# Optimization experiments

Hardware: AMD Instinct MI355X
Metric: run time of the kernel (lower is better)

The kernel has to match this reference:

```python
import jax, jax.numpy as jnp
import numpy as np

ROT_DIM = 32
THETA = 10000.0
HEAD_SIZE = 192


def _rope(t):
    # t: [B, T, D]; rotate first ROT_DIM features with interleaved-pair RoPE
    T = t.shape[1]
    inv_freq = 1.0 / (THETA ** (jnp.arange(0, ROT_DIM, 2, dtype=jnp.float32) / ROT_DIM))  # [16]
    freqs = jnp.arange(T, dtype=jnp.float32)[:, None] * inv_freq[None, :]  # [T,16]
    freqs = jnp.repeat(freqs, 2, axis=-1)  # [T,32], each freq repeated for the pair
    cos = jnp.cos(freqs).astype(t.dtype)
    sin = jnp.sin(freqs).astype(t.dtype)
    x = t[..., :ROT_DIM]
    x1 = x[..., 0::2]
    x2 = x[..., 1::2]
    rot_half = jnp.stack([-x2, x1], axis=-1).reshape(x.shape)  # interleave (-x2, x1)
    rotated = x * cos + rot_half * sin
    return jnp.concatenate([rotated, t[..., ROT_DIM:]], axis=-1)


def setup_inputs() -> dict:
    key = jax.random.key(0)
    k1, k2, k3, k4 = jax.random.split(key, 4)
    B, T, C, H = 64, 512, 768, HEAD_SIZE
    x = jax.random.normal(k1, (B, T, C), dtype=jnp.float32)
    s = 1.0 / np.sqrt(C)
    Wq = jax.random.normal(k2, (C, H), dtype=jnp.float32) * s
    Wk = jax.random.normal(k3, (C, H), dtype=jnp.float32) * s
    Wv = jax.random.normal(k4, (C, H), dtype=jnp.float32) * s
    return {"x": x, "Wq": Wq, "Wk": Wk, "Wv": Wv}


def reference(x, Wq, Wk, Wv):
    B, T, C = x.shape
    q = x @ Wq  # [B,T,H]
    k = x @ Wk
    v = x @ Wv
    q = _rope(q)
    k = _rope(k)
    scale = k.shape[-1] ** -0.5
    scores = jnp.einsum('bqh,bkh->bqk', q, k) * scale  # [B,T,T]
    causal = jnp.tril(jnp.ones((T, T), dtype=bool))
    scores = jnp.where(causal[None, :, :], scores, -jnp.inf)
    weight = jax.nn.softmax(scores, axis=-1)
    # dropout is identity at eval time
    out = jnp.einsum('bqk,bkh->bqh', weight, v)  # [B,T,H]
    return out
```

## Files before the change

kernel.cpp:

```cpp
#include <hip/hip_runtime.h>
#include <cstdint>

typedef __attribute__((ext_vector_type(8))) short short8;
typedef __attribute__((ext_vector_type(4))) float floatx4;

__device__ __forceinline__ unsigned short f2bf(float f) {
  uint32_t u = __builtin_bit_cast(uint32_t, f);
  u += 0x7fffu + ((u >> 16) & 1u);
  return (unsigned short)(u >> 16);
}
__device__ __forceinline__ uint32_t pkbf(float lo, float hi) {
  uint32_t a = __builtin_bit_cast(uint32_t, lo) + 0x8000u;
  uint32_t b = __builtin_bit_cast(uint32_t, hi) + 0x8000u;
  return __builtin_amdgcn_perm(b, a, 0x07060302);
}
__device__ __forceinline__ void gll16(const void* g, void* l) {
  __builtin_amdgcn_global_load_lds(
      (const __attribute__((address_space(1))) unsigned int*)g,
      (__attribute__((address_space(3))) unsigned int*)l, 16, 0, 0);
}

__global__ void prep_w_kernel(const float* __restrict__ Wq,
                              const float* __restrict__ Wk,
                              const float* __restrict__ Wv,
                              unsigned short* __restrict__ Wt) {
  int id = blockIdx.x * 256 + threadIdx.x;
  int bz = id / 18432, rem = id - bz * 18432;
  int kb = rem / 768, s = rem - kb * 768;
  int row = s >> 2, cs = s & 3;
  int c = cs ^ ((row >> 1) & 3);
  const float* W = (bz == 0) ? Wq : (bz == 1) ? Wk : Wv;
  int k0 = kb * 32 + c * 8;
  unsigned short v[8];
#pragma unroll
  for (int e = 0; e < 8; ++e) v[e] = f2bf(W[(size_t)(k0 + e) * 192 + row]);
  uint4 o;
  o.x = v[0] | ((uint32_t)v[1] << 16);
  o.y = v[2] | ((uint32_t)v[3] << 16);
  o.z = v[4] | ((uint32_t)v[5] << 16);
  o.w = v[6] | ((uint32_t)v[7] << 16);
  *(uint4*)(Wt + (size_t)id * 8) = o;
}

__global__ __launch_bounds__(256, 3) void proj_kernel(
    const float* __restrict__ x, const unsigned short* __restrict__ Wt,
    unsigned short* __restrict__ q_ws, unsigned short* __restrict__ k_ws,
    unsigned short* __restrict__ v_ws) {
  __shared__ __align__(16) unsigned short A_lds[3][64 * 32];
  __shared__ __align__(16) unsigned short B_lds[3][192 * 32];
  const int tid = threadIdx.x;
  const int w = tid >> 6, l = tid & 63, quad = l >> 4, ln = l & 15;
  const int wr = w & 1, wc = w >> 1;
  const int m0 = blockIdx.x * 64;
  const int bz = blockIdx.y;

  const int arow = tid >> 2, ac = tid & 3;
  const int aslot = ((ac ^ ((arow >> 1) & 3)) << 4);
  const float* xp = x + (size_t)(m0 + arow) * 768 + ac * 8;
  const unsigned short* wimg = Wt + (size_t)bz * 18432 * 8;

  const int fq = ((quad ^ ((ln >> 1) & 3)) << 4);

  floatx4 acc[2][6];
#pragma unroll
  for (int mi = 0; mi < 2; ++mi)
#pragma unroll
    for (int nj = 0; nj < 6; ++nj) acc[mi][nj] = floatx4{0.f, 0.f, 0.f, 0.f};

  float4 ax0, ay0, ax1, ay1, ax2, ay2;

#define LOADA(S, K0)                               \
  do {                                             \
    ax##S = *(const float4*)(xp + (K0));           \
    ay##S = *(const float4*)(xp + (K0) + 4);       \
  } while (0)
#define STAGEA(S, AB)                                             \
  do {                                                            \
    uint4 ap;                                                     \
    ap.x = pkbf(ax##S.x, ax##S.y);                                \
    ap.y = pkbf(ax##S.z, ax##S.w);                                \
    ap.z = pkbf(ay##S.x, ay##S.y);                                \
    ap.w = pkbf(ay##S.z, ay##S.w);                                \
    *(uint4*)((char*)&A_lds[AB][0] + arow * 64 + aslot) = ap;     \
  } while (0)
#define DMAB(KB1, BB)                                             \
  do {                                                            \
    const unsigned short* src = wimg + (size_t)(KB1)*6144;        \
    char* dstb = (char*)&B_lds[BB][0];                            \
    gll16(src + tid * 8, dstb + tid * 16);                        \
    gll16(src + (256 + tid) * 8, dstb + (256 + tid) * 16);        \
    gll16(src + (512 + tid) * 8, dstb + (512 + tid) * 16);        \
  } while (0)
#define WAITBAR(N)                                                          \
  asm volatile("s_waitcnt vmcnt(" #N ") lgkmcnt(0)\n\ts_barrier" ::: "memory")
#define PCOMPUTE(C)                                                              \
  do {                                                                           \
    short8 af0 = *(const short8*)((const char*)&A_lds[C][0] +                    \
                                  (wr * 32 + ln) * 64 + fq);                     \
    short8 af1 = *(const short8*)((const char*)&A_lds[C][0] +                    \
                                  (wr * 32 + 16 + ln) * 64 + fq);                \
    _Pragma("unroll") for (int nj = 0; nj < 6; ++nj) {                           \
      short8 bf = *(const short8*)((const char*)&B_lds[C][0] +                   \
                                   (wc * 96 + nj * 16 + ln) * 64 + fq);          \
      acc[0][nj] = __builtin_amdgcn_mfma_f32_16x16x32_bf16(af0, bf, acc[0][nj],  \
                                                           0, 0, 0);             \
      acc[1][nj] = __builtin_amdgcn_mfma_f32_16x16x32_bf16(af1, bf, acc[1][nj],  \
                                                           0, 0, 0);             \
    }                                                                            \
  } while (0)
#define BODY(KB, C, P)            \
  do {                            \
    STAGEA(P, P);                 \
    DMAB((KB) + 1, P);            \
    LOADA(C, ((KB) + 3) * 32);    \
    WAITBAR(7);                   \
    PCOMPUTE(C);                  \
  } while (0)

  DMAB(0, 0);
  LOADA(0, 0);
  LOADA(1, 32);
  LOADA(2, 64);
  STAGEA(0, 0);

  BODY(0, 0, 1);
  for (int t = 1; t <= 16; t += 3) {
    BODY(t, 1, 2);
    BODY(t + 1, 2, 0);
    BODY(t + 2, 0, 1);
  }
  BODY(19, 1, 2);
  BODY(20, 2, 0);
  { STAGEA(1, 1); DMAB(22, 1); WAITBAR(5); PCOMPUTE(0); }
  { STAGEA(2, 2); DMAB(23, 2); WAITBAR(3); PCOMPUTE(1); }
  { WAITBAR(0); PCOMPUTE(2); }

#undef LOADA
#undef STAGEA
#undef DMAB
#undef WAITBAR
#undef PCOMPUTE
#undef BODY

  const float R_LG = 0.8304820237218406f;
#define ROPE2(V0, V1, TPOS)                                         \
  do {                                                              \
    float i0 = (float)(ln >> 1);                                    \
    float f0 = exp2f(-i0 * R_LG);                                   \
    float f1 = exp2f(-(i0 + 8.0f) * R_LG);                          \
    float s0, c0, s1, c1;                                           \
    sincosf((float)(TPOS)*f0, &s0, &c0);                            \
    sincosf((float)(TPOS)*f1, &s1, &c1);                            \
    float p0 = __shfl_xor(V0, 1), p1 = __shfl_xor(V1, 1);           \
    V0 = (ln & 1) ? (V0 * c0 + p0 * s0) : (V0 * c0 - p0 * s0);      \
    V1 = (ln & 1) ? (V1 * c1 + p1 * s1) : (V1 * c1 - p1 * s1);      \
  } while (0)

  if (bz < 2) {
    unsigned short* dst = (bz == 0) ? q_ws : k_ws;
    if (wc == 0) {
#pragma unroll
      for (int mi = 0; mi < 2; ++mi)
#pragma unroll
        for (int r = 0; r < 4; ++r) {
          int row_g = m0 + wr * 32 + mi * 16 + quad * 4 + r;
          int t_pos = row_g & 511;
          float v0 = acc[mi][0][r], v1 = acc[mi][1][r];
          ROPE2(v0, v1, t_pos);
          dst[(size_t)row_g * 192 + ln] = f2bf(v0);
          dst[(size_t)row_g * 192 + 16 + ln] = f2bf(v1);
#pragma unroll
          for (int nj = 2; nj < 6; ++nj)
            dst[(size_t)row_g * 192 + nj * 16 + ln] = f2bf(acc[mi][nj][r]);
        }
    } else {
#pragma unroll
      for (int mi = 0; mi < 2; ++mi)
#pragma unroll
        for (int r = 0; r < 4; ++r) {
          int row_g = m0 + wr * 32 + mi * 16 + quad * 4 + r;
#pragma unroll
          for (int nj = 0; nj < 6; ++nj)
            dst[(size_t)row_g * 192 + 96 + nj * 16 + ln] = f2bf(acc[mi][nj][r]);
        }
    }
  } else {
    const int dbase = wc * 96;
#pragma unroll
    for (int mi = 0; mi < 2; ++mi) {
      int rb = m0 + wr * 32 + mi * 16 + quad * 4;
      int bb = rb >> 9, t = rb & 511;
#pragma unroll
      for (int nj = 0; nj < 6; ++nj) {
        ushort4 pv;
        pv.x = f2bf(acc[mi][nj][0]);
        pv.y = f2bf(acc[mi][nj][1]);
        pv.z = f2bf(acc[mi][nj][2]);
        pv.w = f2bf(acc[mi][nj][3]);
        *(ushort4*)&v_ws[((size_t)bb * 192 + dbase + nj * 16 + ln) * 512 + t] = pv;
      }
    }
  }
#undef ROPE2
}

__global__ __launch_bounds__(256) void attn_kernel(
    const unsigned short* __restrict__ q_ws, const unsigned short* __restrict__ k_ws,
    const unsigned short* __restrict__ v_ws, float* __restrict__ out) {
  __shared__ __align__(16) unsigned short K_lds[64 * 200];
  __shared__ __align__(16) unsigned short V_lds[192 * 72];
  __shared__ __align__(16) unsigned short P_lds[4][16 * 72];
  const int tid = threadIdx.x;
  const int w = tid >> 6, l = tid & 63, quad = l >> 4, ln = l & 15;
  const int b = blockIdx.y;
  const int qt = (blockIdx.y < 32) ? blockIdx.x : 7 - blockIdx.x;
  const int q0 = qt * 64;

  short8 qf[6];
  {
    const unsigned short* qp =
        q_ws + (size_t)(b * 512 + q0 + w * 16 + ln) * 192 + quad * 8;
#pragma unroll
    for (int kk = 0; kk < 6; ++kk) qf[kk] = *(const short8*)(qp + kk * 32);
  }

  float m_i[4], l_i[4];
  floatx4 o[12];
#pragma unroll
  for (int r = 0; r < 4; ++r) { m_i[r] = -1e30f; l_i[r] = 0.f; }
#pragma unroll
  for (int nt = 0; nt < 12; ++nt) o[nt] = floatx4{0.f, 0.f, 0.f, 0.f};
  const float sm_scale = 0.07216878364870323f;

  for (int kt = 0; kt <= qt; ++kt) {
    const int k0 = kt * 64;
    __syncthreads();
#pragma unroll
    for (int it = 0; it < 6; ++it) {
      int idx = it * 256 + tid;
      int row = idx / 24, c = idx - row * 24;
      uint4 v = *(const uint4*)(k_ws + (size_t)(b * 512 + k0 + row) * 192 + c * 8);
      *(uint4*)&K_lds[row * 200 + c * 8] = v;
    }
#pragma unroll
    for (int it = 0; it < 6; ++it) {
      int idx = it * 256 + tid;
      int row = idx >> 3, c = idx & 7;
      uint4 v = *(const uint4*)(v_ws + (size_t)(b * 192 + row) * 512 + k0 + c * 8);
      *(uint4*)&V_lds[row * 72 + c * 8] = v;
    }
    __syncthreads();

    float s[4][4];
    __builtin_amdgcn_s_setprio(1);
#pragma unroll
    for (int nt = 0; nt < 4; ++nt) {
      floatx4 sa = floatx4{0.f, 0.f, 0.f, 0.f};
#pragma unroll
      for (int kk = 0; kk < 6; ++kk) {
        short8 kf = *(const short8*)&K_lds[(nt * 16 + ln) * 200 + kk * 32 + quad * 8];
        sa = __builtin_amdgcn_mfma_f32_16x16x32_bf16(qf[kk], kf, sa, 0, 0, 0);
      }
#pragma unroll
      for (int r = 0; r < 4; ++r) s[nt][r] = sa[r] * sm_scale;
    }
    __builtin_amdgcn_s_setprio(0);
    if (kt == qt) {
#pragma unroll
      for (int nt = 0; nt < 4; ++nt)
#pragma unroll
        for (int r = 0; r < 4; ++r)
          if (nt * 16 + ln > w * 16 + quad * 4 + r) s[nt][r] = -1e30f;
    }
    float alpha[4];
#pragma unroll
    for (int r = 0; r < 4; ++r) {
      float mx = fmaxf(fmaxf(s[0][r], s[1][r]), fmaxf(s[2][r], s[3][r]));
      mx = fmaxf(mx, __shfl_xor(mx, 1));
      mx = fmaxf(mx, __shfl_xor(mx, 2));
      mx = fmaxf(mx, __shfl_xor(mx, 4));
      mx = fmaxf(mx, __shfl_xor(mx, 8));
      float mnew = fmaxf(m_i[r], mx);
      alpha[r] = __expf(m_i[r] - mnew);
      float sum = 0.f;
#pragma unroll
      for (int nt = 0; nt < 4; ++nt) {
        s[nt][r] = __expf(s[nt][r] - mnew);
        sum += s[nt][r];
      }
      sum += __shfl_xor(sum, 1);
      sum += __shfl_xor(sum, 2);
      sum += __shfl_xor(sum, 4);
      sum += __shfl_xor(sum, 8);
      l_i[r] = l_i[r] * alpha[r] + sum;
      m_i[r] = mnew;
    }
#pragma unroll
    for (int nt = 0; nt < 12; ++nt)
#pragma unroll
      for (int r = 0; r < 4; ++r) o[nt][r] *= alpha[r];

#pragma unroll
    for (int nt = 0; nt < 4; ++nt)
#pragma unroll
      for (int r = 0; r < 4; ++r)
        P_lds[w][(quad * 4 + r) * 72 + nt * 16 + ln] = f2bf(s[nt][r]);
    __asm__ volatile("s_waitcnt lgkmcnt(0)" ::: "memory");

    __builtin_amdgcn_s_setprio(1);
#pragma unroll
    for (int ks = 0; ks < 2; ++ks) {
      short8 pf = *(const short8*)&P_lds[w][ln * 72 + ks * 32 + quad * 8];
#pragma unroll
      for (int nt = 0; nt < 12; ++nt) {
        short8 vf = *(const short8*)&V_lds[(nt * 16 + ln) * 72 + ks * 32 + quad * 8];
        o[nt] = __builtin_amdgcn_mfma_f32_16x16x32_bf16(pf, vf, o[nt], 0, 0, 0);
      }
    }
    __builtin_amdgcn_s_setprio(0);
  }

#pragma unroll
  for (int r = 0; r < 4; ++r) {
    float inv = 1.0f / l_i[r];
    size_t rowoff = (size_t)(b * 512 + q0 + w * 16 + quad * 4 + r) * 192;
#pragma unroll
    for (int nt = 0; nt < 12; ++nt)
      out[rowoff + nt * 16 + ln] = o[nt][r] * inv;
  }
}

extern "C" void kernel_launch(void* const* d_in, const int* in_sizes, int n_in,
                              void* d_out, int out_size, void* d_ws, size_t ws_size,
                              hipStream_t stream) {
  const float* x = (const float*)d_in[0];
  const float* Wq = (const float*)d_in[1];
  const float* Wk = (const float*)d_in[2];
  const float* Wv = (const float*)d_in[3];
  float* out = (float*)d_out;

  char* ws = (char*)d_ws;
  const size_t QKV_BYTES = (size_t)64 * 512 * 192 * 2;
  unsigned short* q_ws = (unsigned short*)(ws);
  unsigned short* k_ws = (unsigned short*)(ws + QKV_BYTES);
  unsigned short* v_ws = (unsigned short*)(ws + 2 * QKV_BYTES);
  unsigned short* Wt = (unsigned short*)(ws + 3 * QKV_BYTES);

  hipLaunchKernelGGL(prep_w_kernel, dim3(216), dim3(256), 0, stream, Wq, Wk, Wv, Wt);
  hipLaunchKernelGGL(proj_kernel, dim3(512, 3), dim3(256), 0, stream, x, Wt, q_ws, k_ws, v_ws);
  hipLaunchKernelGGL(attn_kernel, dim3(8, 64), dim3(256), 0, stream, q_ws, k_ws, v_ws, out);
}
```

Measured before the change: 222.5 us.

## Pre-convert x to bf16 for DMA projection and shrink attention key tile to 32

Adds a prep kernel that converts x to bf16 once. A new projection kernel then streams both operands straight into LDS with global_load_lds, in place of register-staged fp32 loads that are converted inside the main loop. This path runs only when the workspace is large enough, and it adds an extra pass over x plus a bf16 copy. Separately, the attention kernel now uses 32-key tiles instead of 64, which halves LDS use and lets the causal diagonal skip finer-grained work, at the cost of twice as many loop iterations and barriers.

New measurement: 236.2 us. 6.2% more time.

```diff
diff --git a/kernel.cpp b/kernel.cpp
--- a/kernel.cpp
+++ b/kernel.cpp
@@ -42,6 +42,151 @@
   *(uint4*)(Wt + (size_t)id * 8) = o;
 }
 
+__global__ void prep_x_kernel(const float* __restrict__ x,
+                              unsigned short* __restrict__ xb) {
+  size_t id = (size_t)blockIdx.x * 256 + threadIdx.x;
+  float4 f0 = *(const float4*)(x + id * 8);
+  float4 f1 = *(const float4*)(x + id * 8 + 4);
+  uint4 o;
+  o.x = pkbf(f0.x, f0.y);
+  o.y = pkbf(f0.z, f0.w);
+  o.z = pkbf(f1.x, f1.y);
+  o.w = pkbf(f1.z, f1.w);
+  *(uint4*)(xb + id * 8) = o;
+}
+
+#define PROJ_EPILOGUE                                                          \
+  const float R_LG = 0.8304820237218406f;                  \
+  if (bz < 2) {                                                                \
+    unsigned short* dst = (bz == 0) ? q_ws : k_ws;                             \
+    if (wc == 0) {                                                             \
+      _Pragma("unroll") for (int mi = 0; mi < 2; ++mi)                         \
+      _Pragma("unroll") for (int r = 0; r < 4; ++r) {                          \
+        int row_g = m0 + wr * 32 + mi * 16 + quad * 4 + r;                     \
+        int t_pos = row_g & 511;                                               \
+        float v0 = acc[mi][0][r], v1 = acc[mi][1][r];                          \
+        {                                                                      \
+          float i0 = (float)(ln >> 1);                                         \
+          float f0 = exp2f(-i0 * R_LG);                                        \
+          float f1 = exp2f(-(i0 + 8.0f) * R_LG);                               \
+          float s0, c0, s1, c1;                                                \
+          sincosf((float)t_pos * f0, &s0, &c0);                                \
+          sincosf((float)t_pos * f1, &s1, &c1);                                \
+          float p0 = __shfl_xor(v0, 1), p1 = __shfl_xor(v1, 1);                \
+          v0 = (ln & 1) ? (v0 * c0 + p0 * s0) : (v0 * c0 - p0 * s0);           \
+          v1 = (ln & 1) ? (v1 * c1 + p1 * s1) : (v1 * c1 - p1 * s1);           \
+        }                                                                      \
+        dst[(size_t)row_g * 192 + ln] = f2bf(v0);                              \
+        dst[(size_t)row_g * 192 + 16 + ln] = f2bf(v1);                         \
+        _Pragma("unroll") for (int nj = 2; nj < 6; ++nj)                       \
+            dst[(size_t)row_g * 192 + nj * 16 + ln] = f2bf(acc[mi][nj][r]);    \
+      }                                                                        \
+    } else {                                                                   \
+      _Pragma("unroll") for (int mi = 0; mi < 2; ++mi)                         \
+      _Pragma("unroll") for (int r = 0; r < 4; ++r) {                          \
+        int row_g = m0 + wr * 32 + mi * 16 + quad * 4 + r;                     \
+        _Pragma("unroll") for (int nj = 0; nj < 6; ++nj)                       \
+            dst[(size_t)row_g * 192 + 96 + nj * 16 + ln] =                     \
+                f2bf(acc[mi][nj][r]);                                          \
+      }                                                                        \
+    }                                                                          \
+  } else {                                                                     \
+    const int dbase = wc * 96;                                                 \
+    _Pragma("unroll") for (int mi = 0; mi < 2; ++mi) {                         \
+      int rb = m0 + wr * 32 + mi * 16 + quad * 4;                              \
+      int bb = rb >> 9, t = rb & 511;                                          \
+      _Pragma("unroll") for (int nj = 0; nj < 6; ++nj) {                       \
+        ushort4 pv;                                                            \
+        pv.x = f2bf(acc[mi][nj][0]);                                           \
+        pv.y = f2bf(acc[mi][nj][1]);                                           \
+        pv.z = f2bf(acc[mi][nj][2]);                                           \
+        pv.w = f2bf(acc[mi][nj][3]);                                           \
+        *(ushort4*)&v_ws[((size_t)bb * 192 + dbase + nj * 16 + ln) * 512 + t] = pv; \
+      }                                                                        \
+    }                                                                          \
+  }
+
+__global__ __launch_bounds__(256, 3) void proj_dma_kernel(
+    const unsigned short* __restrict__ xb, const unsigned short* __restrict__ Wt,
+    unsigned short* __restrict__ q_ws, unsigned short* __restrict__ k_ws,
+    unsigned short* __restrict__ v_ws) {
+  __shared__ __align__(16) unsigned short A_lds[3][64 * 32];
+  __shared__ __align__(16) unsigned short B_lds[3][192 * 32];
+  const int tid = threadIdx.x;
+  const int w = tid >> 6, l = tid & 63, quad = l >> 4, ln = l & 15;
+  const int wr = w & 1, wc = w >> 1;
+  const int m0 = blockIdx.x * 64;
+  const int bz = blockIdx.y;
+
+  const int arow = tid >> 2, ac = tid & 3;
+  const int aswz = ac ^ ((arow >> 1) & 3);
+  const unsigned short* xsrc = xb + (size_t)(m0 + arow) * 768 + aswz * 8;
+  const unsigned short* wimg = Wt + (size_t)bz * 18432 * 8;
+
+  const int fq = ((quad ^ ((ln >> 1) & 3)) << 4);
+
+  floatx4 acc[2][6];
+#pragma unroll
+  for (int mi = 0; mi < 2; ++mi)
+#pragma unroll
+    for (int nj = 0; nj < 6; ++nj) acc[mi][nj] = floatx4{0.f, 0.f, 0.f, 0.f};
+
+#define DMAA(KB, BB) gll16(xsrc + (KB) * 32, (char*)&A_lds[BB][0] + tid * 16)
+#define DMAB(KB, BB)                                                  \
+  do {                                                                \
+    const unsigned short* src = wimg + (size_t)(KB)*6144;             \
+    char* dstb = (char*)&B_lds[BB][0];                                \
+    gll16(src + tid * 8, dstb + tid * 16);                            \
+    gll16(src + (256 + tid) * 8, dstb + (256 + tid) * 16);            \
+    gll16(src + (512 + tid) * 8, dstb + (512 + tid) * 16);            \
+  } while (0)
+#define WAITBAR4 \
+  asm volatile("s_waitcnt vmcnt(4) lgkmcnt(0)\n\ts_barrier" ::: "memory")
+#define WAITBAR0 \
+  asm volatile("s_waitcnt vmcnt(0) lgkmcnt(0)\n\ts_barrier" ::: "memory")
+#define PCOMPUTE(C)                                                              \
+  do {                                                                           \
+    short8 af0 = *(const short8*)((const char*)&A_lds[C][0] +                    \
+                                  (wr * 32 + ln) * 64 + fq);                     \
+    short8 af1 = *(const short8*)((const char*)&A_lds[C][0] +                    \
+                                  (wr * 32 + 16 + ln) * 64 + fq);                \
+    _Pragma("unroll") for (int nj = 0; nj < 6; ++nj) {                           \
+      short8 bf = *(const short8*)((const char*)&B_lds[C][0] +                   \
+                                   (wc * 96 + nj * 16 + ln) * 64 + fq);          \
+      acc[0][nj] = __builtin_amdgcn_mfma_f32_16x16x32_bf16(af0, bf, acc[0][nj],  \
+                                                           0, 0, 0);             \
+      acc[1][nj] = __builtin_amdgcn_mfma_f32_16x16x32_bf16(af1, bf, acc[1][nj],  \
+                                                           0, 0, 0);             \
+    }                                                                            \
+  } while (0)
+#define BODY(J, C, N)                                   \
+  do {                                                  \
+    DMAA((J) + 1, N);                                   \
+    DMAB((J) + 1, N);                                   \
+    WAITBAR4;                                           \
+    PCOMPUTE(C);                                        \
+  } while (0)
+
+  DMAA(0, 0);
+  DMAB(0, 0);
+  BODY(0, 0, 1);
+  for (int t = 1; t <= 19; t += 3) {
+    BODY(t, 1, 2);
+    BODY(t + 1, 2, 0);
+    BODY(t + 2, 0, 1);
+  }
+  BODY(22, 1, 2);
+  { WAITBAR0; PCOMPUTE(2); }
+#undef DMAA
+#undef DMAB
+#undef WAITBAR4
+#undef WAITBAR0
+#undef PCOMPUTE
+#undef BODY
+
+  PROJ_EPILOGUE
+}
+
 __global__ __launch_bounds__(256, 3) void proj_kernel(
     const float* __restrict__ x, const unsigned short* __restrict__ Wt,
     unsigned short* __restrict__ q_ws, unsigned short* __restrict__ k_ws,
@@ -58,7 +203,6 @@
   const int aslot = ((ac ^ ((arow >> 1) & 3)) << 4);
   const float* xp = x + (size_t)(m0 + arow) * 768 + ac * 8;
   const unsigned short* wimg = Wt + (size_t)bz * 18432 * 8;
-
   const int fq = ((quad ^ ((ln >> 1) & 3)) << 4);
 
   floatx4 acc[2][6];
@@ -134,7 +278,6 @@
   { STAGEA(1, 1); DMAB(22, 1); WAITBAR(5); PCOMPUTE(0); }
   { STAGEA(2, 2); DMAB(23, 2); WAITBAR(3); PCOMPUTE(1); }
   { WAITBAR(0); PCOMPUTE(2); }
-
 #undef LOADA
 #undef STAGEA
 #undef DMAB
@@ -142,74 +285,15 @@
 #undef PCOMPUTE
 #undef BODY
 
-  const float R_LG = 0.8304820237218406f;
-#define ROPE2(V0, V1, TPOS)                                         \
-  do {                                                              \
-    float i0 = (float)(ln >> 1);                                    \
-    float f0 = exp2f(-i0 * R_LG);                                   \
-    float f1 = exp2f(-(i0 + 8.0f) * R_LG);                          \
-    float s0, c0, s1, c1;                                           \
-    sincosf((float)(TPOS)*f0, &s0, &c0);                            \
-    sincosf((float)(TPOS)*f1, &s1, &c1);                            \
-    float p0 = __shfl_xor(V0, 1), p1 = __shfl_xor(V1, 1);           \
-    V0 = (ln & 1) ? (V0 * c0 + p0 * s0) : (V0 * c0 - p0 * s0);      \
-    V1 = (ln & 1) ? (V1 * c1 + p1 * s1) : (V1 * c1 - p1 * s1);      \
-  } while (0)
-
-  if (bz < 2) {
-    unsigned short* dst = (bz == 0) ? q_ws : k_ws;
-    if (wc == 0) {
-#pragma unroll
-      for (int mi = 0; mi < 2; ++mi)
-#pragma unroll
-        for (int r = 0; r < 4; ++r) {
-          int row_g = m0 + wr * 32 + mi * 16 + quad * 4 + r;
-          int t_pos = row_g & 511;
-          float v0 = acc[mi][0][r], v1 = acc[mi][1][r];
-          ROPE2(v0, v1, t_pos);
-          dst[(size_t)row_g * 192 + ln] = f2bf(v0);
-          dst[(size_t)row_g * 192 + 16 + ln] = f2bf(v1);
-#pragma unroll
-          for (int nj = 2; nj < 6; ++nj)
-            dst[(size_t)row_g * 192 + nj * 16 + ln] = f2bf(acc[mi][nj][r]);
-        }
-    } else {
-#pragma unroll
-      for (int mi = 0; mi < 2; ++mi)
-#pragma unroll
-        for (int r = 0; r < 4; ++r) {
-          int row_g = m0 + wr * 32 + mi * 16 + quad * 4 + r;
-#pragma unroll
-          for (int nj = 0; nj < 6; ++nj)
-            dst[(size_t)row_g * 192 + 96 + nj * 16 + ln] = f2bf(acc[mi][nj][r]);
-        }
-    }
-  } else {
-    const int dbase = wc * 96;
-#pragma unroll
-    for (int mi = 0; mi < 2; ++mi) {
-      int rb = m0 + wr * 32 + mi * 16 + quad * 4;
-      int bb = rb >> 9, t = rb & 511;
-#pragma unroll
-      for (int nj = 0; nj < 6; ++nj) {
-        ushort4 pv;
-        pv.x = f2bf(acc[mi][nj][0]);
-        pv.y = f2bf(acc[mi][nj][1]);
-        pv.z = f2bf(acc[mi][nj][2]);
-        pv.w = f2bf(acc[mi][nj][3]);
-        *(ushort4*)&v_ws[((size_t)bb * 192 + dbase + nj * 16 + ln) * 512 + t] = pv;
-      }
-    }
-  }
-#undef ROPE2
+  PROJ_EPILOGUE
 }
 
 __global__ __launch_bounds__(256) void attn_kernel(
     const unsigned short* __restrict__ q_ws, const unsigned short* __restrict__ k_ws,
     const unsigned short* __restrict__ v_ws, float* __restrict__ out) {
-  __shared__ __align__(16) unsigned short K_lds[64 * 200];
-  __shared__ __align__(16) unsigned short V_lds[192 * 72];
-  __shared__ __align__(16) unsigned short P_lds[4][16 * 72];
+  __shared__ __align__(16) unsigned short K_lds[32 * 200];
+  __shared__ __align__(16) unsigned short V_lds[192 * 40];
+  __shared__ __align__(16) unsigned short P_lds[4][16 * 40];
   const int tid = threadIdx.x;
   const int w = tid >> 6, l = tid & 63, quad = l >> 4, ln = l & 15;
   const int b = blockIdx.y;
@@ -232,29 +316,30 @@
   for (int nt = 0; nt < 12; ++nt) o[nt] = floatx4{0.f, 0.f, 0.f, 0.f};
   const float sm_scale = 0.07216878364870323f;
 
-  for (int kt = 0; kt <= qt; ++kt) {
-    const int k0 = kt * 64;
+  const int ktmax = 2 * qt + 1;
+  for (int kt = 0; kt <= ktmax; ++kt) {
+    const int k0 = kt * 32;
     __syncthreads();
 #pragma unroll
-    for (int it = 0; it < 6; ++it) {
+    for (int it = 0; it < 3; ++it) {
       int idx = it * 256 + tid;
       int row = idx / 24, c = idx - row * 24;
       uint4 v = *(const uint4*)(k_ws + (size_t)(b * 512 + k0 + row) * 192 + c * 8);
       *(uint4*)&K_lds[row * 200 + c * 8] = v;
     }
 #pragma unroll
-    for (int it = 0; it < 6; ++it) {
+    for (int it = 0; it < 3; ++it) {
       int idx = it * 256 + tid;
-      int row = idx >> 3, c = idx & 7;
+      int row = idx >> 2, c = idx & 3;
       uint4 v = *(const uint4*)(v_ws + (size_t)(b * 192 + row) * 512 + k0 + c * 8);
-      *(uint4*)&V_lds[row * 72 + c * 8] = v;
+      *(uint4*)&V_lds[row * 40 + c * 8] = v;
     }
     __syncthreads();
 
-    float s[4][4];
+    float s[2][4];
     __builtin_amdgcn_s_setprio(1);
 #pragma unroll
-    for (int nt = 0; nt < 4; ++nt) {
+    for (int nt = 0; nt < 2; ++nt) {
       floatx4 sa = floatx4{0.f, 0.f, 0.f, 0.f};
 #pragma unroll
       for (int kk = 0; kk < 6; ++kk) {
@@ -265,17 +350,18 @@
       for (int r = 0; r < 4; ++r) s[nt][r] = sa[r] * sm_scale;
     }
     __builtin_amdgcn_s_setprio(0);
-    if (kt == qt) {
-#pragma unroll
-      for (int nt = 0; nt < 4; ++nt)
+    if (kt >= 2 * qt) {
+      int kd = (kt - 2 * qt) * 32;
+#pragma unroll
+      for (int nt = 0; nt < 2; ++nt)
 #pragma unroll
         for (int r = 0; r < 4; ++r)
-          if (nt * 16 + ln > w * 16 + quad * 4 + r) s[nt][r] = -1e30f;
+          if (kd + nt * 16 + ln > w * 16 + quad * 4 + r) s[nt][r] = -1e30f;
     }
     float alpha[4];
 #pragma unroll
     for (int r = 0; r < 4; ++r) {
-      float mx = fmaxf(fmaxf(s[0][r], s[1][r]), fmaxf(s[2][r], s[3][r]));
+      float mx = fmaxf(s[0][r], s[1][r]);
       mx = fmaxf(mx, __shfl_xor(mx, 1));
       mx = fmaxf(mx, __shfl_xor(mx, 2));
       mx = fmaxf(mx, __shfl_xor(mx, 4));
@@ -284,7 +370,7 @@
       alpha[r] = __expf(m_i[r] - mnew);
       float sum = 0.f;
 #pragma unroll
-      for (int nt = 0; nt < 4; ++nt) {
+      for (int nt = 0; nt < 2; ++nt) {
         s[nt][r] = __expf(s[nt][r] - mnew);
         sum += s[nt][r];
       }
@@ -301,19 +387,18 @@
       for (int r = 0; r < 4; ++r) o[nt][r] *= alpha[r];
 
 #pragma unroll
-    for (int nt = 0; nt < 4; ++nt)
+    for (int nt = 0; nt < 2; ++nt)
 #pragma unroll
       for (int r = 0; r < 4; ++r)
-        P_lds[w][(quad * 4 + r) * 72 + nt * 16 + ln] = f2bf(s[nt][r]);
+        P_lds[w][(quad * 4 + r) * 40 + nt * 16 + ln] = f2bf(s[nt][r]);
     __asm__ volatile("s_waitcnt lgkmcnt(0)" ::: "memory");
 
     __builtin_amdgcn_s_setprio(1);
-#pragma unroll
-    for (int ks = 0; ks < 2; ++ks) {
-      short8 pf = *(const short8*)&P_lds[w][ln * 72 + ks * 32 + quad * 8];
+    {
+      short8 pf = *(const short8*)&P_lds[w][ln * 40 + quad * 8];
 #pragma unroll
       for (int nt = 0; nt < 12; ++nt) {
-        short8 vf = *(const short8*)&V_lds[(nt * 16 + ln) * 72 + ks * 32 + quad * 8];
+        short8 vf = *(const short8*)&V_lds[(nt * 16 + ln) * 40 + quad * 8];
         o[nt] = __builtin_amdgcn_mfma_f32_16x16x32_bf16(pf, vf, o[nt], 0, 0, 0);
       }
     }
@@ -341,12 +426,24 @@
 
   char* ws = (char*)d_ws;
   const size_t QKV_BYTES = (size_t)64 * 512 * 192 * 2;
+  const size_t WT_BYTES = (size_t)55296 * 16;
+  const size_t XBF_BYTES = (size_t)32768 * 768 * 2;
   unsigned short* q_ws = (unsigned short*)(ws);
   unsigned short* k_ws = (unsigned short*)(ws + QKV_BYTES);
   unsigned short* v_ws = (unsigned short*)(ws + 2 * QKV_BYTES);
   unsigned short* Wt = (unsigned short*)(ws + 3 * QKV_BYTES);
+  unsigned short* xb = (unsigned short*)(ws + 3 * QKV_BYTES + WT_BYTES);
+
+  const bool big = ws_size >= 3 * QKV_BYTES + WT_BYTES + XBF_BYTES;
 
   hipLaunchKernelGGL(prep_w_kernel, dim3(216), dim3(256), 0, stream, Wq, Wk, Wv, Wt);
-  hipLaunchKernelGGL(proj_kernel, dim3(512, 3), dim3(256), 0, stream, x, Wt, q_ws, k_ws, v_ws);
+  if (big) {
+    hipLaunchKernelGGL(prep_x_kernel, dim3(12288), dim3(256), 0, stream, x, xb);
+    hipLaunchKernelGGL(proj_dma_kernel, dim3(512, 3), dim3(256), 0, stream, xb, Wt,
+                       q_ws, k_ws, v_ws);
+  } else {
+    hipLaunchKernelGGL(proj_kernel, dim3(512, 3), dim3(256), 0, stream, x, Wt,
+                       q_ws, k_ws, v_ws);
+  }
   hipLaunchKernelGGL(attn_kernel, dim3(8, 64), dim3(256), 0, stream, q_ws, k_ws, v_ws, out);
 }
```
